# Kernel optimization log

Measured on AMD Instinct MI355X. Metric: run time of the kernel, lower is better.

Reference implementation:

```python
import jax, jax.numpy as jnp
import numpy as np

B, N, F, K, H = 2, 1024, 64, 8, 4
M1 = K + 1                # 9
M2 = (F - 1) * K + 1      # 505
TEMP = 1.0


def setup_inputs() -> dict:
    key = jax.random.key(0)
    ks = jax.random.split(key, 8)
    x = jax.random.normal(ks[0], (B, N, F), dtype=jnp.float32)
    # Bernoulli(0.05) dense adjacency
    adj = (jax.random.uniform(ks[1], (B, N, N)) < 0.05).astype(jnp.float32)
    mask = jnp.ones((B, N), dtype=jnp.float32)
    Wl = jax.random.normal(ks[2], (F, K * H), dtype=jnp.float32) * 0.05
    bl = jnp.zeros((K * H,), dtype=jnp.float32)
    Wr = jax.random.normal(ks[3], (F, K * H), dtype=jnp.float32) * 0.05
    br = jnp.zeros((K * H,), dtype=jnp.float32)
    # fixed affine layer: y = x @ aff_w + aff_b, aff_w[:, :F] = -I, aff_b[M2] = 1
    aff_w = jnp.zeros((F, M1 * M2), dtype=jnp.float32).at[:, :F].set(-jnp.eye(F, dtype=jnp.float32))
    aff_b = jnp.zeros((M1 * M2,), dtype=jnp.float32).at[M2].set(1.0)
    Wm = jax.random.normal(ks[4], (M1 * M2, F), dtype=jnp.float32) * 0.02
    bm = jnp.zeros((F,), dtype=jnp.float32)
    return dict(x=x, adj=adj, mask=mask, Wl=Wl, bl=bl, Wr=Wr, br=br,
                aff_w=aff_w, aff_b=aff_b, Wm=Wm, bm=bm)


def reference(x, adj, mask, Wl, bl, Wr, br, aff_w, aff_b, Wm, bm):
    # --- multi-head edge attention ---
    x_l = (x @ Wl + bl).reshape(B, N, K, H)   # [B,N,K,H]
    x_r = (x @ Wr + br).reshape(B, N, K, H)
    # scores[b,i,j,n,g] = leaky_relu(x_l[b,j] + x_r[b,i]) / temp
    scores = jax.nn.leaky_relu(x_l[:, None, :, :, :] + x_r[:, :, None, :, :]) / TEMP  # [B,N,N,K,H]
    attn_mask = mask[:, None, :] * mask[:, :, None]                # [B,N,N]
    scores = jnp.where(attn_mask[..., None, None] == 0, -1e9, scores)
    att = jax.nn.softmax(scores, axis=2)                           # softmax over source nodes j
    att = jnp.maximum(att * adj[..., None, None], 1e-6)            # clamp(min=1e-6) STE trick
    att = att / jnp.sum(att, axis=2, keepdims=True)                # renormalize
    # --- attention-weighted neighbor gather ---
    x_h = x.reshape(B, N, H, F // H)
    agg = jnp.einsum('bjgk,bijng->bingk', x_h, att).reshape(B, N, K, F)  # [B,N,K,F]
    # --- fixed affine + FFT log-domain geometric mean ---
    x_aff = (agg @ aff_w + aff_b).reshape(B, N, K, M1, M2)
    x_fft = jnp.fft.fft2(x_aff)                                    # over (M1,M2)
    mag = jnp.exp(jnp.mean(jnp.log(jnp.abs(x_fft) + 1e-6), axis=2))  # [B,N,M1,M2]
    ang = jnp.sum(jnp.angle(x_fft), axis=2)
    x_agg = jnp.fft.ifft2(mag * jnp.exp(1j * ang)).real.reshape(B, N, M1 * M2)
    # --- output MLP + node mask ---
    out = x_agg @ Wm + bm
    return out * mask[..., None]
```

## Files before the change

kernel.cpp:

```cpp
#include <hip/hip_runtime.h>
#include <math.h>

#define NN 1024
#define FD 64
#define CH 32
#define M1D 9
#define M2D 505
#define QH 253
#define THALF 2273
#define KPAD 4608
#define KSPLIT 16
#define KCHUNK 288
#define G1SZ 291456
#define G1KS 8

#define FSQRT(x) __builtin_amdgcn_sqrtf(x)
#define FRCP(x)  __builtin_amdgcn_rcpf(x)

typedef short short8 __attribute__((ext_vector_type(8)));
typedef float f32x4 __attribute__((ext_vector_type(4)));

__device__ __forceinline__ unsigned short f2bf(float x) {
    unsigned int u = __builtin_bit_cast(unsigned int, x);
    return (unsigned short)((u + 0x7FFFu + ((u >> 16) & 1u)) >> 16);
}

#define OFF_WP    1024
#define OFF_SUMX  1056
#define OFF_GMT   1184
#define OFF_XL    148640
#define OFF_XR    214176
#define OFF_AGG   279712
#define OFF_PART  1328288
#define OFF_Y     3425440
#define OFF_WT    8144032
#define OFF_G1P   8176800

__global__ __launch_bounds__(256) void build_tw_kernel(float* __restrict__ T,
                                                       float* __restrict__ Wt,
                                                       float* __restrict__ wp,
                                                       float* __restrict__ sumx) {
    int idx = blockIdx.x * 256 + threadIdx.x;
    if (blockIdx.x == 0) {
        if (threadIdx.x < M1D) {
            float ang = (float)threadIdx.x * (-6.2831853f / 9.0f);
            float s, c; __sincosf(ang, &s, &c);
            wp[2*threadIdx.x] = c; wp[2*threadIdx.x+1] = s;
        }
        if (threadIdx.x >= 64 && threadIdx.x < 192) sumx[threadIdx.x - 64] = 0.f;
    }
    if (idx < 506 * 512) {
        int r = idx >> 9, m2 = idx & 511;
        float v = 0.f;
        if (m2 < M2D) {
            int q = r >> 1;
            int t = (q * m2) % M2D;
            float ang = (float)t * (-6.2831853f / 505.0f);
            float s, c; __sincosf(ang, &s, &c);
            v = (r & 1) ? -s : c;
        }
        T[idx] = v;
    } else if (idx < 506 * 512 + 64 * 512) {
        int i2 = idx - 506 * 512;
        int m = i2 >> 9, col = i2 & 511;
        float v = 0.f;
        if (col < 506) {
            int q = col >> 1;
            int t = (q * m) % M2D;
            float ang = (float)t * (-6.2831853f / 505.0f);
            float s, c; __sincosf(ang, &s, &c);
            v = (col & 1) ? s : c;
        }
        Wt[i2] = v;
    }
}

__global__ __launch_bounds__(64) void proj_kernel(const float* __restrict__ x,
                                                  const float* __restrict__ Wl, const float* __restrict__ bl,
                                                  const float* __restrict__ Wr, const float* __restrict__ br,
                                                  float* __restrict__ xl, float* __restrict__ xr,
                                                  float* __restrict__ sumx) {
    int blk = blockIdx.x, tid = threadIdx.x;
    if (blk >= 2048) {
        int bb = blk - 2048;
        int b = bb >> 4, chunk = bb & 15;
        const float* xb = x + (size_t)b * NN * FD;
        float acc = 0.f;
        int j0 = chunk * 64;
        #pragma unroll 4
        for (int j = j0; j < j0 + 64; j++) acc += xb[j*FD + tid];
        atomicAdd(&sumx[b*FD + tid], acc);
        return;
    }
    int node = blk;
    __shared__ float xrow[FD];
    xrow[tid] = x[(size_t)node*FD + tid];
    __syncthreads();
    int c = tid & 31;
    const float* W = (tid < 32) ? Wl : Wr;
    float acc = (tid < 32) ? bl[c] : br[c];
    #pragma unroll
    for (int f = 0; f < FD; f++) acc += xrow[f] * W[f*CH + c];
    float* dst = (tid < 32) ? xl : xr;
    dst[(size_t)node*CH + c] = acc;
}

__global__ __launch_bounds__(256) void g1_gemm_kernel(const float* __restrict__ T,
                                                      const float* __restrict__ Wm,
                                                      float* __restrict__ G1p) {
    int mt = blockIdx.x, m1 = blockIdx.y, ks = blockIdx.z;
    int tid = threadIdx.x;
    __shared__ float As[64][68];
    __shared__ float Bs[64][64];
    int r0 = mt * 64, k0 = ks * 64;
    const float* Wmb = Wm + (size_t)m1 * M2D * FD;
    float ra[16], rb[16];
    #pragma unroll
    for (int i = 0; i < 16; i++) {
        int l = tid + i*256;
        int r = l >> 6, k = l & 63;
        int rr = r0 + r;
        ra[i] = (rr < 506) ? T[(size_t)rr*512 + k0 + k] : 0.f;
    }
    #pragma unroll
    for (int i = 0; i < 16; i++) {
        int l = tid + i*256;
        int k = l >> 6, f = l & 63;
        int krow = k0 + k;
        rb[i] = (krow < M2D) ? Wmb[(size_t)krow*FD + f] : 0.f;
    }
    #pragma unroll
    for (int i = 0; i < 16; i++) {
        int l = tid + i*256;
        As[l & 63][l >> 6] = ra[i];
    }
    #pragma unroll
    for (int i = 0; i < 16; i++) {
        int l = tid + i*256;
        Bs[l >> 6][l & 63] = rb[i];
    }
    __syncthreads();
    float acc[4][4] = {{0.f}};
    int tm = (tid >> 4) * 4, tf = (tid & 15) * 4;
    #pragma unroll 8
    for (int k = 0; k < 64; k++) {
        float4 a = *(const float4*)&As[k][tm];
        float4 b = *(const float4*)&Bs[k][tf];
        acc[0][0] += a.x*b.x; acc[0][1] += a.x*b.y; acc[0][2] += a.x*b.z; acc[0][3] += a.x*b.w;
        acc[1][0] += a.y*b.x; acc[1][1] += a.y*b.y; acc[1][2] += a.y*b.z; acc[1][3] += a.y*b.w;
        acc[2][0] += a.z*b.x; acc[2][1] += a.z*b.y; acc[2][2] += a.z*b.z; acc[2][3] += a.z*b.w;
        acc[3][0] += a.w*b.x; acc[3][1] += a.w*b.y; acc[3][2] += a.w*b.z; acc[3][3] += a.w*b.w;
    }
    float* G1k = G1p + (size_t)ks * G1SZ;
    #pragma unroll
    for (int i = 0; i < 4; i++) {
        int r = r0 + tm + i;
        if (r >= 506) continue;
        int q = r >> 1, reim = r & 1;
        size_t base = (size_t)(m1*QH + q) * 128;
        #pragma unroll
        for (int j = 0; j < 4; j++)
            G1k[base + (tf + j)*2 + reim] = acc[i][j];
    }
}

__global__ __launch_bounds__(64) void gmat_kernel(const float* __restrict__ G1p,
                                                  const float* __restrict__ wp,
                                                  unsigned short* __restrict__ GmT) {
    int t = blockIdx.x;
    int f = threadIdx.x;
    if (t >= THALF) {
        *(unsigned int*)&GmT[(size_t)f*KPAD + 2*t] = 0u;
        return;
    }
    int p, q;
    if (t < QH) { p = 0; q = t; }
    else { int u = t - QH; p = 1 + u / M2D; q = u % M2D; }
    int qq = (q < QH) ? q : (M2D - q);
    float sgn = (q < QH) ? 1.f : -1.f;
    float gr = 0.f, gi = 0.f;
    #pragma unroll
    for (int m1 = 0; m1 < M1D; m1++) {
        size_t o = ((size_t)(m1*QH + qq)*FD + f)*2;
        float ar = 0.f, ai = 0.f;
        #pragma unroll
        for (int ks = 0; ks < G1KS; ks++) {
            ar += G1p[(size_t)ks*G1SZ + o];
            ai += G1p[(size_t)ks*G1SZ + o + 1];
        }
        ai *= sgn;
        int pm = (p * m1) % M1D;
        float cr = wp[2*pm], ci = -wp[2*pm+1];
        gr += ar*cr - ai*ci;
        gi += ar*ci + ai*cr;
    }
    float scale = (t == 0) ? (1.0f/4545.0f) : (2.0f/4545.0f);
    unsigned int pk = (unsigned int)f2bf(gr*scale) | ((unsigned int)f2bf(-gi*scale) << 16);
    *(unsigned int*)&GmT[(size_t)f*KPAD + 2*t] = pk;
}

__global__ __launch_bounds__(256) void attn_agg_kernel(const float* __restrict__ x,
                                                       const float* __restrict__ adj,
                                                       const float* __restrict__ xl,
                                                       const float* __restrict__ xr,
                                                       const float* __restrict__ sumx,
                                                       float* __restrict__ agg) {
    int node = blockIdx.x;
    int b = node >> 10;
    int tid = threadIdx.x;
    __shared__ float xr_s[CH], Zinv[CH], Sinv[CH];
    __shared__ float red16[16][CH];
    __shared__ int act_list[NN + 8];
    __shared__ int act_n;
    __shared__ float qv2[64][CH];

    if (tid < CH) xr_s[tid] = xr[(size_t)node*CH + tid];
    if (tid == 0) act_n = 0;
    __syncthreads();

    int c = tid & 31, jl = tid >> 5;
    const float* xlb = xl + ((size_t)b << 10) * CH;
    const float* adjrow = adj + (size_t)node * NN;

    int c2 = tid & 15, jl16 = tid >> 4;
    const float2* xlb2 = (const float2*)xlb;
    float xrcx = xr_s[2*c2], xrcy = xr_s[2*c2+1];
    float zx = 0.f, zy = 0.f;
    for (int j0 = jl16; j0 < NN; j0 += 128) {
        float2 sv[8];
        #pragma unroll
        for (int u = 0; u < 8; u++) sv[u] = xlb2[(size_t)(j0 + u*16)*16 + c2];
        #pragma unroll
        for (int u = 0; u < 8; u++) {
            float s0 = sv[u].x + xrcx; s0 = s0 > 0.f ? s0 : 0.01f * s0;
            float s1 = sv[u].y + xrcy; s1 = s1 > 0.f ? s1 : 0.01f * s1;
            zx += __expf(s0); zy += __expf(s1);
        }
    }
    red16[jl16][2*c2]   = zx;
    red16[jl16][2*c2+1] = zy;

    float av[4];
    #pragma unroll
    for (int u = 0; u < 4; u++) av[u] = adjrow[tid + u*256];
    __syncthreads();
    if (tid < CH) {
        float z = 0.f;
        #pragma unroll
        for (int r = 0; r < 16; r++) z += red16[r][tid];
        Zinv[tid] = FRCP(z);
    }
    #pragma unroll
    for (int u = 0; u < 4; u++)
        if (av[u] != 0.f) { int p = atomicAdd(&act_n, 1); act_list[p] = tid + u*256; }
    __syncthreads();
    int nact = act_n;

    int f = tid & 63, n0 = tid >> 6;
    int g = f >> 4;
    int c0 = n0*4 + g, c1 = (n0+4)*4 + g;
    const float* xb = x + ((size_t)b << 10) * FD;
    float acc0 = 0.f, acc1 = 0.f, sacc = 0.f;

    for (int base = 0; base < nact; base += 64) {
        int cnt = min(64, nact - base);
        int cntp = (cnt + 7) & ~7;
        for (int u = tid; u < (cnt << 5); u += 256) {
            int jj = u >> 5, cc = u & 31;
            int j = act_list[base + jj];
            float s = xlb[j*CH + cc] + xr_s[cc];
            s = s > 0.f ? s : 0.01f * s;
            float pv = __expf(s) * Zinv[cc];
            float qq = fmaxf(pv, 1e-6f) - 1e-6f;
            qv2[jj][cc] = qq;
            sacc += qq;
        }
        for (int u = tid + (cnt << 5); u < (cntp << 5); u += 256)
            qv2[u >> 5][u & 31] = 0.f;
        if (tid < cntp - cnt) act_list[base + cnt + tid] = act_list[base];
        __syncthreads();
        for (int jb = 0; jb < cntp; jb += 8) {
            float xv[8];
            #pragma unroll
            for (int u = 0; u < 8; u++) xv[u] = xb[act_list[base + jb + u]*FD + f];
            #pragma unroll
            for (int u = 0; u < 8; u++) {
                acc0 += qv2[jb+u][c0] * xv[u];
                acc1 += qv2[jb+u][c1] * xv[u];
            }
        }
        __syncthreads();
    }
    red16[jl][c] = sacc;
    __syncthreads();
    if (tid < CH) {
        float s = 0.f;
        #pragma unroll
        for (int r = 0; r < 8; r++) s += red16[r][tid];
        Sinv[tid] = FRCP(s + (float)NN * 1e-6f);
    }
    __syncthreads();
    float sx = sumx[b*FD + f] * 1e-6f;
    agg[(size_t)node*512 + n0*FD + f]       = (acc0 + sx) * Sinv[c0];
    agg[(size_t)node*512 + (n0+4)*FD + f]   = (acc1 + sx) * Sinv[c1];
}

__global__ __launch_bounds__(256) void ay_kernel(const float* __restrict__ agg,
                                                 const float* __restrict__ Wt,
                                                 unsigned short* __restrict__ Yb) {
    int slab = blockIdx.x, nt = blockIdx.y;
    int tid = threadIdx.x;
    __shared__ float As2[64][68];
    __shared__ float Bs[64][64];
    int tm = (tid >> 4) * 4, tf = (tid & 15) * 4;
    float ra[16], rb[16];
    #pragma unroll
    for (int i = 0; i < 16; i++) {
        int l = tid + i*256;
        int r = l >> 6, k = l & 63;
        ra[i] = agg[(size_t)(slab*64 + r)*64 + k];
    }
    #pragma unroll
    for (int i = 0; i < 16; i++) {
        int l = tid + i*256;
        int k = l >> 6, cc = l & 63;
        rb[i] = Wt[(size_t)k*512 + nt*64 + cc];
    }
    #pragma unroll
    for (int i = 0; i < 16; i++) { int l = tid + i*256; As2[l & 63][l >> 6] = ra[i]; }
    #pragma unroll
    for (int i = 0; i < 16; i++) { int l = tid + i*256; Bs[l >> 6][l & 63] = rb[i]; }
    __syncthreads();
    float acc[4][4] = {{0.f}};
    #pragma unroll 8
    for (int k = 0; k < 64; k++) {
        float4 a = *(const float4*)&As2[k][tm];
        float4 b = *(const float4*)&Bs[k][tf];
        acc[0][0] += a.x*b.x; acc[0][1] += a.x*b.y; acc[0][2] += a.x*b.z; acc[0][3] += a.x*b.w;
        acc[1][0] += a.y*b.x; acc[1][1] += a.y*b.y; acc[1][2] += a.y*b.z; acc[1][3] += a.y*b.w;
        acc[2][0] += a.z*b.x; acc[2][1] += a.z*b.y; acc[2][2] += a.z*b.z; acc[2][3] += a.z*b.w;
        acc[3][0] += a.w*b.x; acc[3][1] += a.w*b.y; acc[3][2] += a.w*b.z; acc[3][3] += a.w*b.w;
    }
    __syncthreads();
    #pragma unroll
    for (int i = 0; i < 4; i++)
        #pragma unroll
        for (int j = 0; j < 4; j++)
            As2[tm + i][tf + j] = acc[i][j];
    __syncthreads();

    int qloc = tid & 31, node = tid >> 5;
    unsigned short* Yrow = Yb + (size_t)(slab*8 + node)*KPAD;
    int q = nt*32 + qloc;

    if (q <= 252) {
        float2 Av[8];
        #pragma unroll
        for (int n = 0; n < 8; n++)
            Av[n] = make_float2(As2[node*8 + n][2*qloc], As2[node*8 + n][2*qloc + 1]);

        const float CPt[5] = {1.0f, 0.766044443119f, 0.173648177667f, -0.5f, -0.939692620786f};
        const float SPt[5] = {0.0f, -0.642787609687f, -0.984807753012f, -0.866025403784f, -0.342020143326f};

        #define Y_PROD(CSIGN, TIDX)                                            \
        {                                                                      \
            float Pr = 1.f, Pi = 0.f, rp2 = 1.f;                               \
            _Pragma("unroll")                                                  \
            for (int n = 0; n < 8; n++) {                                      \
                float Xr = cp - Av[n].x, Xi = sp - (CSIGN) * Av[n].y;          \
                rp2 *= (Xr*Xr + Xi*Xi);                                        \
                float nPr = Pr*Xr - Pi*Xi;                                     \
                Pi = Pr*Xi + Pi*Xr; Pr = nPr;                                  \
            }                                                                  \
            float pAbs = FSQRT(Pr*Pr + Pi*Pi);                                 \
            float rp8 = FSQRT(FSQRT(FSQRT(FSQRT(rp2))));                       \
            float s = rp8 * FRCP(fmaxf(pAbs, 1e-20f));                         \
            unsigned int pk = (unsigned int)f2bf(s*Pr) | ((unsigned int)f2bf(s*Pi) << 16); \
            *(unsigned int*)&Yrow[2*(TIDX)] = pk;                              \
        }

        #pragma unroll
        for (int p = 0; p < 5; p++) {
            float cp = CPt[p], sp = SPt[p];
            int tfwd = (p == 0) ? q : (QH + (p-1)*M2D + q);
            Y_PROD(1.f, tfwd);
            if (p >= 1 && q >= 1) {
                int tmir = QH + (p-1)*M2D + (M2D - q);
                Y_PROD(-1.f, tmir);
            }
        }
        #undef Y_PROD
    }
    if (nt == 7 && tid < 248) {
        int rr = tid / 31, cc2 = tid % 31;
        unsigned short* Yr2 = Yb + (size_t)(slab*8 + rr)*KPAD;
        *(unsigned int*)&Yr2[2*THALF + 2*cc2] = 0u;
    }
}

__global__ __launch_bounds__(256) void gemm_kernel(const unsigned short* __restrict__ Yb,
                                                   const unsigned short* __restrict__ GmT,
                                                   float* __restrict__ part) {
    int mtile = blockIdx.x, kc = blockIdx.y;
    int tid = threadIdx.x;
    __shared__ unsigned short Ys[64*40];
    __shared__ unsigned short Gs[64*40];
    int m0 = mtile * 64;
    int k0 = kc * KCHUNK;
    int r = tid >> 2, kg = (tid & 3) * 8;
    const unsigned short* Ysrc = Yb + (size_t)(m0 + r)*KPAD + k0 + kg;
    const unsigned short* Gsrc = GmT + (size_t)r*KPAD + k0 + kg;
    uint4 ya = *(const uint4*)Ysrc;
    uint4 ga = *(const uint4*)Gsrc;
    int w = tid >> 6, lane = tid & 63;
    int lm = lane & 15, quad = lane >> 4;
    f32x4 acc0 = {0.f,0.f,0.f,0.f}, acc1 = acc0, acc2 = acc0, acc3 = acc0;
    for (int ks = 0; ks < KCHUNK; ks += 32) {
        *(uint4*)&Ys[r*40 + kg] = ya;
        *(uint4*)&Gs[r*40 + kg] = ga;
        __syncthreads();
        if (ks + 32 < KCHUNK) {
            ya = *(const uint4*)(Ysrc + ks + 32);
            ga = *(const uint4*)(Gsrc + ks + 32);
        }
        short8 b  = *(const short8*)&Gs[(w*16 + lm)*40 + quad*8];
        short8 a0 = *(const short8*)&Ys[(lm)*40      + quad*8];
        short8 a1 = *(const short8*)&Ys[(16 + lm)*40 + quad*8];
        short8 a2 = *(const short8*)&Ys[(32 + lm)*40 + quad*8];
        short8 a3 = *(const short8*)&Ys[(48 + lm)*40 + quad*8];
        acc0 = __builtin_amdgcn_mfma_f32_16x16x32_bf16(a0, b, acc0, 0, 0, 0);
        acc1 = __builtin_amdgcn_mfma_f32_16x16x32_bf16(a1, b, acc1, 0, 0, 0);
        acc2 = __builtin_amdgcn_mfma_f32_16x16x32_bf16(a2, b, acc2, 0, 0, 0);
        acc3 = __builtin_amdgcn_mfma_f32_16x16x32_bf16(a3, b, acc3, 0, 0, 0);
        __syncthreads();
    }
    float* prow = part + (size_t)kc * (2048*FD);
    int col = w*16 + lm;
    #pragma unroll
    for (int rr = 0; rr < 4; rr++) {
        int row = quad*4 + rr;
        prow[(size_t)(m0 + row)*FD + col]      = acc0[rr];
        prow[(size_t)(m0 + 16 + row)*FD + col] = acc1[rr];
        prow[(size_t)(m0 + 32 + row)*FD + col] = acc2[rr];
        prow[(size_t)(m0 + 48 + row)*FD + col] = acc3[rr];
    }
}

__global__ __launch_bounds__(256) void reduce_kernel(const float* __restrict__ part,
                                                     const float* __restrict__ bm,
                                                     const float* __restrict__ mask,
                                                     float* __restrict__ out) {
    int idx = blockIdx.x * 256 + threadIdx.x;
    if (idx >= 32768) return;
    const float4* p4 = (const float4*)part;
    float4 s = p4[idx];
    #pragma unroll
    for (int kc = 1; kc < KSPLIT; kc++) {
        float4 v = p4[(size_t)kc*32768 + idx];
        s.x += v.x; s.y += v.y; s.z += v.z; s.w += v.w;
    }
    int f0 = (idx & 15) * 4;
    int node = idx >> 4;
    float mk = mask[node];
    s.x = (s.x + bm[f0])   * mk;
    s.y = (s.y + bm[f0+1]) * mk;
    s.z = (s.z + bm[f0+2]) * mk;
    s.w = (s.w + bm[f0+3]) * mk;
    ((float4*)out)[idx] = s;
}

extern "C" void kernel_launch(void* const* d_in, const int* in_sizes, int n_in,
                              void* d_out, int out_size, void* d_ws, size_t ws_size,
                              hipStream_t stream) {
    const float* x    = (const float*)d_in[0];
    const float* adj  = (const float*)d_in[1];
    const float* mask = (const float*)d_in[2];
    const float* Wl   = (const float*)d_in[3];
    const float* bl   = (const float*)d_in[4];
    const float* Wr   = (const float*)d_in[5];
    const float* br   = (const float*)d_in[6];
    const float* Wm   = (const float*)d_in[9];
    const float* bm   = (const float*)d_in[10];
    float* out = (float*)d_out;
    float* ws  = (float*)d_ws;

    float* wp   = ws + OFF_WP;
    float* sumx = ws + OFF_SUMX;
    unsigned short* GmT = (unsigned short*)(ws + OFF_GMT);
    float* xl   = ws + OFF_XL;
    float* xr   = ws + OFF_XR;
    float* agg  = ws + OFF_AGG;
    float* part = ws + OFF_PART;
    float* T    = ws + OFF_Y;
    unsigned short* Yb = (unsigned short*)(ws + OFF_Y);
    float* Wt   = ws + OFF_WT;
    float* G1p  = ws + OFF_G1P;

    hipLaunchKernelGGL(build_tw_kernel, dim3((506*512 + 64*512 + 255)/256), dim3(256), 0, stream, T, Wt, wp, sumx);
    hipLaunchKernelGGL(proj_kernel, dim3(2080), dim3(64), 0, stream, x, Wl, bl, Wr, br, xl, xr, sumx);
    hipLaunchKernelGGL(g1_gemm_kernel, dim3(8, 9, G1KS), dim3(256), 0, stream, T, Wm, G1p);
    hipLaunchKernelGGL(gmat_kernel, dim3(KPAD/2), dim3(64), 0, stream, G1p, wp, GmT);
    hipLaunchKernelGGL(attn_agg_kernel, dim3(2048), dim3(256), 0, stream, x, adj, xl, xr, sumx, agg);
    hipLaunchKernelGGL(ay_kernel, dim3(256, 8), dim3(256), 0, stream, agg, Wt, Yb);
    hipLaunchKernelGGL(gemm_kernel, dim3(32, KSPLIT), dim3(256), 0, stream, Yb, GmT, part);
    hipLaunchKernelGGL(reduce_kernel, dim3(128), dim3(256), 0, stream, part, bm, mask, out);
}
```

Before: 177.8 us.

## Split softmax denominator into separate kernel computing four nodes per block

```diff
diff --git a/kernel.cpp b/kernel.cpp
--- a/kernel.cpp
+++ b/kernel.cpp
@@ -35,6 +35,7 @@
 #define OFF_Y     3425440
 #define OFF_WT    8144032
 #define OFF_G1P   8176800
+#define OFF_ZG    10508448
 
 __global__ __launch_bounds__(256) void build_tw_kernel(float* __restrict__ T,
                                                        float* __restrict__ Wt,
@@ -105,6 +106,51 @@
     dst[(size_t)node*CH + c] = acc;
 }
 
+__global__ __launch_bounds__(256) void z4_kernel(const float* __restrict__ xl,
+                                                 const float* __restrict__ xr,
+                                                 float* __restrict__ Zg) {
+    int node0 = blockIdx.x * 4;
+    int b = node0 >> 10;
+    int tid = threadIdx.x;
+    int c2 = tid & 15, jl16 = tid >> 4;
+    __shared__ float red[16][128];
+    const float2* xlb2 = (const float2*)(xl + (((size_t)b) << 10) * CH);
+    float xrx[4], xry[4];
+    #pragma unroll
+    for (int v = 0; v < 4; v++) {
+        const float* xrn = xr + (size_t)(node0 + v) * CH;
+        xrx[v] = xrn[2*c2]; xry[v] = xrn[2*c2+1];
+    }
+    float zx[4] = {0.f,0.f,0.f,0.f}, zy[4] = {0.f,0.f,0.f,0.f};
+    for (int j0 = jl16; j0 < NN; j0 += 128) {
+        float2 sv[8];
+        #pragma unroll
+        for (int u = 0; u < 8; u++) sv[u] = xlb2[(size_t)(j0 + u*16)*16 + c2];
+        #pragma unroll
+        for (int u = 0; u < 8; u++) {
+            #pragma unroll
+            for (int v = 0; v < 4; v++) {
+                float s0 = sv[u].x + xrx[v]; s0 = s0 > 0.f ? s0 : 0.01f * s0;
+                float s1 = sv[u].y + xry[v]; s1 = s1 > 0.f ? s1 : 0.01f * s1;
+                zx[v] += __expf(s0); zy[v] += __expf(s1);
+            }
+        }
+    }
+    #pragma unroll
+    for (int v = 0; v < 4; v++) {
+        red[jl16][v*32 + 2*c2]   = zx[v];
+        red[jl16][v*32 + 2*c2+1] = zy[v];
+    }
+    __syncthreads();
+    if (tid < 128) {
+        float z = 0.f;
+        #pragma unroll
+        for (int r = 0; r < 16; r++) z += red[r][tid];
+        int v = tid >> 5, c = tid & 31;
+        Zg[(size_t)(node0 + v)*CH + c] = FRCP(z);
+    }
+}
+
 __global__ __launch_bounds__(256) void g1_gemm_kernel(const float* __restrict__ T,
                                                       const float* __restrict__ Wm,
                                                       float* __restrict__ G1p) {
@@ -203,59 +249,36 @@
                                                        const float* __restrict__ adj,
                                                        const float* __restrict__ xl,
                                                        const float* __restrict__ xr,
+                                                       const float* __restrict__ Zg,
                                                        const float* __restrict__ sumx,
                                                        float* __restrict__ agg) {
     int node = blockIdx.x;
     int b = node >> 10;
     int tid = threadIdx.x;
     __shared__ float xr_s[CH], Zinv[CH], Sinv[CH];
-    __shared__ float red16[16][CH];
+    __shared__ float red[8][CH];
     __shared__ int act_list[NN + 8];
     __shared__ int act_n;
     __shared__ float qv2[64][CH];
 
-    if (tid < CH) xr_s[tid] = xr[(size_t)node*CH + tid];
+    if (tid < CH) {
+        xr_s[tid] = xr[(size_t)node*CH + tid];
+        Zinv[tid] = Zg[(size_t)node*CH + tid];
+    }
     if (tid == 0) act_n = 0;
-    __syncthreads();
+    const float* adjrow = adj + (size_t)node * NN;
+    float av[4];
+    #pragma unroll
+    for (int u = 0; u < 4; u++) av[u] = adjrow[tid + u*256];
+    __syncthreads();
+    #pragma unroll
+    for (int u = 0; u < 4; u++)
+        if (av[u] != 0.f) { int p = atomicAdd(&act_n, 1); act_list[p] = tid + u*256; }
+    __syncthreads();
+    int nact = act_n;
 
     int c = tid & 31, jl = tid >> 5;
     const float* xlb = xl + ((size_t)b << 10) * CH;
-    const float* adjrow = adj + (size_t)node * NN;
-
-    int c2 = tid & 15, jl16 = tid >> 4;
-    const float2* xlb2 = (const float2*)xlb;
-    float xrcx = xr_s[2*c2], xrcy = xr_s[2*c2+1];
-    float zx = 0.f, zy = 0.f;
-    for (int j0 = jl16; j0 < NN; j0 += 128) {
-        float2 sv[8];
-        #pragma unroll
-        for (int u = 0; u < 8; u++) sv[u] = xlb2[(size_t)(j0 + u*16)*16 + c2];
-        #pragma unroll
-        for (int u = 0; u < 8; u++) {
-            float s0 = sv[u].x + xrcx; s0 = s0 > 0.f ? s0 : 0.01f * s0;
-            float s1 = sv[u].y + xrcy; s1 = s1 > 0.f ? s1 : 0.01f * s1;
-            zx += __expf(s0); zy += __expf(s1);
-        }
-    }
-    red16[jl16][2*c2]   = zx;
-    red16[jl16][2*c2+1] = zy;
-
-    float av[4];
-    #pragma unroll
-    for (int u = 0; u < 4; u++) av[u] = adjrow[tid + u*256];
-    __syncthreads();
-    if (tid < CH) {
-        float z = 0.f;
-        #pragma unroll
-        for (int r = 0; r < 16; r++) z += red16[r][tid];
-        Zinv[tid] = FRCP(z);
-    }
-    #pragma unroll
-    for (int u = 0; u < 4; u++)
-        if (av[u] != 0.f) { int p = atomicAdd(&act_n, 1); act_list[p] = tid + u*256; }
-    __syncthreads();
-    int nact = act_n;
-
     int f = tid & 63, n0 = tid >> 6;
     int g = f >> 4;
     int c0 = n0*4 + g, c1 = (n0+4)*4 + g;
@@ -291,12 +314,12 @@
         }
         __syncthreads();
     }
-    red16[jl][c] = sacc;
+    red[jl][c] = sacc;
     __syncthreads();
     if (tid < CH) {
         float s = 0.f;
         #pragma unroll
-        for (int r = 0; r < 8; r++) s += red16[r][tid];
+        for (int r = 0; r < 8; r++) s += red[r][tid];
         Sinv[tid] = FRCP(s + (float)NN * 1e-6f);
     }
     __syncthreads();
@@ -495,12 +518,14 @@
     unsigned short* Yb = (unsigned short*)(ws + OFF_Y);
     float* Wt   = ws + OFF_WT;
     float* G1p  = ws + OFF_G1P;
+    float* Zg   = ws + OFF_ZG;
 
     hipLaunchKernelGGL(build_tw_kernel, dim3((506*512 + 64*512 + 255)/256), dim3(256), 0, stream, T, Wt, wp, sumx);
     hipLaunchKernelGGL(proj_kernel, dim3(2080), dim3(64), 0, stream, x, Wl, bl, Wr, br, xl, xr, sumx);
+    hipLaunchKernelGGL(z4_kernel, dim3(512), dim3(256), 0, stream, xl, xr, Zg);
     hipLaunchKernelGGL(g1_gemm_kernel, dim3(8, 9, G1KS), dim3(256), 0, stream, T, Wm, G1p);
     hipLaunchKernelGGL(gmat_kernel, dim3(KPAD/2), dim3(64), 0, stream, G1p, wp, GmT);
-    hipLaunchKernelGGL(attn_agg_kernel, dim3(2048), dim3(256), 0, stream, x, adj, xl, xr, sumx, agg);
+    hipLaunchKernelGGL(attn_agg_kernel, dim3(2048), dim3(256), 0, stream, x, adj, xl, xr, Zg, sumx, agg);
     hipLaunchKernelGGL(ay_kernel, dim3(256, 8), dim3(256), 0, stream, agg, Wt, Yb);
     hipLaunchKernelGGL(gemm_kernel, dim3(32, KSPLIT), dim3(256), 0, stream, Yb, GmT, part);
     hipLaunchKernelGGL(reduce_kernel, dim3(128), dim3(256), 0, stream, part, bm, mask, out);
```

Measured after the change: 179.9 us. About the same (+1.2%).
